# Kernel tuning notes

Measured on AMD Instinct MI355X. Metric: run time of the kernel, lower is better.

## Reference

```python
import jax, jax.numpy as jnp
import numpy as np

B, I, H = 16384, 1024, 1024
LN_EPS = 1e-5


def setup_inputs() -> dict:
    key = jax.random.key(0)
    k1, k2, k3, k4 = jax.random.split(key, 4)
    x = jax.random.normal(k1, (B, I), dtype=jnp.float32)
    h_out = jax.random.normal(k2, (B, H), dtype=jnp.float32)
    cell = jax.random.normal(k3, (B, H), dtype=jnp.float32)
    # nn.Linear(i_size + h, 4*h, bias=False): weight shape [4h, i+h]
    W = jax.random.normal(k4, (4 * H, I + H), dtype=jnp.float32) * (1.0 / np.sqrt(I + H))
    gamma = jnp.ones((4, H), dtype=jnp.float32)
    beta = jnp.zeros((4, H), dtype=jnp.float32)
    return {"x": x, "h_out": h_out, "cell": cell, "W": W, "gamma": gamma, "beta": beta}


def reference(x, h_out, cell, W, gamma, beta):
    # concat + linear -> [B, 4, H]
    cat = jnp.concatenate([x, h_out], axis=-1)               # [B, I+H]
    t = (cat @ W.T).reshape(cat.shape[0], 4, H)              # [B, 4, H]
    # LayerNorm over normalized_shape=(4, H): stats over last two dims
    mu = jnp.mean(t, axis=(-2, -1), keepdims=True)
    var = jnp.mean(jnp.square(t - mu), axis=(-2, -1), keepdims=True)
    handle = (t - mu) * jax.lax.rsqrt(var + LN_EPS) * gamma + beta
    # gates: first 3 slices sigmoid, last slice GELU (exact, eval-mode dropout = identity)
    gates = jax.nn.sigmoid(handle[:, 0:3, :])
    f_gate, i_gate, o_gate = gates[:, 0], gates[:, 1], gates[:, 2]
    h_cand = jax.nn.gelu(handle[:, 3, :], approximate=False)
    new_cell = f_gate * cell + i_gate * h_cand
    new_out = o_gate * new_cell
    return (new_out, new_cell)
```

## Files before the change

### kernel.cpp

```cpp
#include <hip/hip_runtime.h>
#include <stdint.h>

#define B_ROWS 16384
#define IN_DIM 1024
#define H_DIM  1024
#define KDIM   2048
#define NDIM   4096
#define NT     64
#define LN_EPSF 1e-5f

typedef unsigned short u16;
typedef float  f32x4  __attribute__((ext_vector_type(4)));
typedef float  fv4    __attribute__((ext_vector_type(4)));
typedef __bf16 bf16x8 __attribute__((ext_vector_type(8)));
typedef u16    u16x4  __attribute__((ext_vector_type(4)));
typedef u16    u16x8  __attribute__((ext_vector_type(8)));

__device__ __forceinline__ u16 f2bf(float f) {
  unsigned u = __float_as_uint(f);
  u += 0x7FFFu + ((u >> 16) & 1u);
  return (u16)(u >> 16);
}
__device__ __forceinline__ float bf2f(u16 s) {
  return __uint_as_float(((unsigned)s) << 16);
}

#define GLOAD_LDS16(gp, lp) __builtin_amdgcn_global_load_lds( \
    (__attribute__((address_space(1))) void*)(gp),            \
    (__attribute__((address_space(3))) void*)(lp), 16, 0, 0)

__global__ __launch_bounds__(256) void cast_concat(
    const float* __restrict__ x, const float* __restrict__ h,
    u16* __restrict__ cat) {
  int idx = blockIdx.x * 256 + threadIdx.x;
  long base = (long)idx * 8;
  int  c = (int)(base & (KDIM - 1));
  long b = base >> 11;
  const float* src = (c < IN_DIM) ? (x + b * IN_DIM + c)
                                  : (h + b * H_DIM + (c - IN_DIM));
  fv4 v0 = *(const fv4*)(src);
  fv4 v1 = *(const fv4*)(src + 4);
  u16x8 o;
  o[0]=f2bf(v0[0]); o[1]=f2bf(v0[1]); o[2]=f2bf(v0[2]); o[3]=f2bf(v0[3]);
  o[4]=f2bf(v1[0]); o[5]=f2bf(v1[1]); o[6]=f2bf(v1[2]); o[7]=f2bf(v1[3]);
  *(u16x8*)(cat + base) = o;
}

__global__ __launch_bounds__(256) void cast_plain(
    const float* __restrict__ w, u16* __restrict__ wb) {
  int idx = blockIdx.x * 256 + threadIdx.x;
  long base = (long)idx * 8;
  fv4 v0 = *(const fv4*)(w + base);
  fv4 v1 = *(const fv4*)(w + base + 4);
  u16x8 o;
  o[0]=f2bf(v0[0]); o[1]=f2bf(v0[1]); o[2]=f2bf(v0[2]); o[3]=f2bf(v0[3]);
  o[4]=f2bf(v1[0]); o[5]=f2bf(v1[1]); o[6]=f2bf(v1[2]); o[7]=f2bf(v1[3]);
  *(u16x8*)(wb + base) = o;
}


#define BODY(J, CA, CB, NA, NB) do {                                         \
    const int t = tb + (J);                                                  \
    const bool st = (t + 3) < NT;                                            \
    const u16* __restrict__ ab  = &As[(J) & 3][0];                           \
    const u16* __restrict__ bb  = &Bs[(J) & 3][0];                           \
    const u16* __restrict__ abn = &As[((J) + 1) & 3][0];                     \
    const u16* __restrict__ bbn = &Bs[((J) + 1) & 3][0];                     \
    u16* __restrict__ sa = &As[((J) + 3) & 3][0];                            \
    u16* __restrict__ sb = &Bs[((J) + 3) & 3][0];                            \
    if (st) {                                                                \
      GLOAD_LDS16(gA0 + (size_t)(t + 3) * 32, sa + tid * 8);                 \
      GLOAD_LDS16(gA1 + (size_t)(t + 3) * 32, sa + tid * 8 + 4096);          \
    }                                                                        \
    _Pragma("unroll")                                                        \
    for (int i = 0; i < 4; ++i)                                              \
      A47[i] = *(const bf16x8*)(ab + base_a + (4 + i) * 512);                \
    __builtin_amdgcn_sched_barrier(0);                                       \
    __builtin_amdgcn_s_setprio(1);                                           \
    _Pragma("unroll")                                                        \
    for (int m = 0; m < 4; ++m)                                              \
      _Pragma("unroll")                                                      \
      for (int n = 0; n < 4; ++n)                                            \
        acc[m][n] = __builtin_amdgcn_mfma_f32_16x16x32_bf16(                 \
            CA[m], CB[n], acc[m][n], 0, 0, 0);                               \
    __builtin_amdgcn_s_setprio(0);                                           \
    __builtin_amdgcn_sched_barrier(0);                                       \
    if (st) {                                                                \
      GLOAD_LDS16(gB0 + (size_t)(t + 3) * 32, sb + tid * 8);                 \
      GLOAD_LDS16(gB1 + (size_t)(t + 3) * 32, sb + tid * 8 + 4096);          \
    }                                                                        \
    if (t + 1 < NT) {                                                        \
      _Pragma("unroll")                                                      \
      for (int i = 0; i < 4; ++i) {                                          \
        NA[i] = *(const bf16x8*)(abn + base_a + i * 512);                    \
        NB[i] = *(const bf16x8*)(bbn + base_b + i * 512);                    \
      }                                                                      \
    }                                                                        \
    __builtin_amdgcn_sched_barrier(0);                                       \
    __builtin_amdgcn_s_setprio(1);                                           \
    _Pragma("unroll")                                                        \
    for (int m = 0; m < 4; ++m)                                              \
      _Pragma("unroll")                                                      \
      for (int n = 0; n < 4; ++n)                                            \
        acc[4 + m][n] = __builtin_amdgcn_mfma_f32_16x16x32_bf16(             \
            A47[m], CB[n], acc[4 + m][n], 0, 0, 0);                          \
    __builtin_amdgcn_s_setprio(0);                                           \
    __builtin_amdgcn_sched_barrier(0);                                       \
    asm volatile("s_waitcnt vmcnt(4)" ::: "memory");                         \
    __builtin_amdgcn_s_barrier();                                            \
  } while (0)

__global__ __launch_bounds__(512, 2) void gemm_bt(
    const u16* __restrict__ A,
    const u16* __restrict__ Bw,
    u16* __restrict__ C) {
  __shared__ u16 As[4][8192];
  __shared__ u16 Bs[4][8192];

  const int tid  = threadIdx.x;
  const int lane = tid & 63;
  const int wave = tid >> 6;
  const int wm   = wave >> 2;
  const int wn   = wave & 3;
  const int r    = lane & 15;
  const int g    = lane >> 4;

  const int bid = blockIdx.x;
  const int xcd = bid & 7;
  const int k_  = bid >> 3;
  const int row0 = (xcd * 8 + (k_ >> 4)) * 256;
  const int col0 = (k_ & 15) * 256;

  const int tid2 = tid ^ ((tid >> 3) & 7);
  const u16* gA0 = A  + (size_t)(row0 + (tid2 >> 2)) * KDIM + (tid2 & 3) * 8;
  const u16* gA1 = gA0 + (size_t)128 * KDIM;
  const u16* gB0 = Bw + (size_t)(col0 + (tid2 >> 2)) * KDIM + (tid2 & 3) * 8;
  const u16* gB1 = gB0 + (size_t)128 * KDIM;

  const int rswz   = ((r >> 1) & 7) << 3;
  const int base_a = (((wm * 128 + r) * 32) + g * 8) ^ rswz;
  const int base_b = (((wn * 64  + r) * 32) + g * 8) ^ rswz;

  f32x4 acc[8][4] = {};
  bf16x8 XA[4], XB[4], YA[4], YB[4], A47[4];

#pragma unroll
  for (int tt = 0; tt < 3; ++tt) {
    GLOAD_LDS16(gA0 + tt * 32, &As[tt][tid * 8]);
    GLOAD_LDS16(gA1 + tt * 32, &As[tt][tid * 8 + 4096]);
    GLOAD_LDS16(gB0 + tt * 32, &Bs[tt][tid * 8]);
    GLOAD_LDS16(gB1 + tt * 32, &Bs[tt][tid * 8 + 4096]);
  }
  asm volatile("s_waitcnt vmcnt(4)" ::: "memory");
  __builtin_amdgcn_s_barrier();
#pragma unroll
  for (int i = 0; i < 4; ++i) {
    XA[i] = *(const bf16x8*)(&As[0][0] + base_a + i * 512);
    XB[i] = *(const bf16x8*)(&Bs[0][0] + base_b + i * 512);
  }

  for (int u = 0; u < 16; ++u) {
    const int tb = u * 4;
    BODY(0, XA, XB, YA, YB);
    BODY(1, YA, YB, XA, XB);
    BODY(2, XA, XB, YA, YB);
    BODY(3, YA, YB, XA, XB);
  }

#pragma unroll
  for (int m = 0; m < 8; ++m)
#pragma unroll
    for (int n = 0; n < 4; ++n)
#pragma unroll
      for (int q = 0; q < 4; ++q) {
        const int rr = row0 + wm * 128 + m * 16 + g * 4 + q;
        const int cc = col0 + wn * 64 + n * 16 + r;
        C[(size_t)rr * NDIM + cc] = f2bf(acc[m][n][q]);
      }
}

__global__ __launch_bounds__(256) void ln_gates(
    const u16* __restrict__ t,
    const float* __restrict__ cell,
    const float* __restrict__ gamma,
    const float* __restrict__ beta,
    float* __restrict__ out) {
  const int b   = blockIdx.x;
  const int tid = threadIdx.x;
  const int h0  = tid * 4;

  const u16* trow = t + (long)b * NDIM;
  float v[4][4];
#pragma unroll
  for (int gi = 0; gi < 4; ++gi) {
    u16x4 raw = *(const u16x4*)&trow[gi * H_DIM + h0];
#pragma unroll
    for (int j = 0; j < 4; ++j) v[gi][j] = bf2f(raw[j]);
  }

  float s1 = 0.f, s2 = 0.f;
#pragma unroll
  for (int gi = 0; gi < 4; ++gi)
#pragma unroll
    for (int j = 0; j < 4; ++j) { s1 += v[gi][j]; s2 += v[gi][j] * v[gi][j]; }

#pragma unroll
  for (int m = 32; m; m >>= 1) {
    s1 += __shfl_xor(s1, m);
    s2 += __shfl_xor(s2, m);
  }
  __shared__ float red[2][4];
  const int wave = tid >> 6, lane = tid & 63;
  if (lane == 0) { red[0][wave] = s1; red[1][wave] = s2; }
  __syncthreads();
  s1 = red[0][0] + red[0][1] + red[0][2] + red[0][3];
  s2 = red[1][0] + red[1][1] + red[1][2] + red[1][3];

  const float mean  = s1 * (1.f / (float)NDIM);
  const float var   = s2 * (1.f / (float)NDIM) - mean * mean;
  const float scale = rsqrtf(var + LN_EPSF);

  float hd[4][4];
#pragma unroll
  for (int gi = 0; gi < 4; ++gi) {
    fv4 gm = *(const fv4*)&gamma[gi * H_DIM + h0];
    fv4 bt = *(const fv4*)&beta[gi * H_DIM + h0];
#pragma unroll
    for (int j = 0; j < 4; ++j)
      hd[gi][j] = (v[gi][j] - mean) * scale * gm[j] + bt[j];
  }

  fv4 cv = *(const fv4*)&cell[(long)b * H_DIM + h0];
  fv4 no, nc;
#pragma unroll
  for (int j = 0; j < 4; ++j) {
    float fg = 1.f / (1.f + expf(-hd[0][j]));
    float ig = 1.f / (1.f + expf(-hd[1][j]));
    float og = 1.f / (1.f + expf(-hd[2][j]));
    float hc = 0.5f * hd[3][j] * (1.f + erff(hd[3][j] * 0.70710678118654752f));
    float ncell = fg * cv[j] + ig * hc;
    nc[j] = ncell;
    no[j] = og * ncell;
  }
  *(fv4*)&out[(long)b * H_DIM + h0] = no;
  *(fv4*)&out[(long)B_ROWS * H_DIM + (long)b * H_DIM + h0] = nc;
}

extern "C" void kernel_launch(void* const* d_in, const int* in_sizes, int n_in,
                              void* d_out, int out_size, void* d_ws, size_t ws_size,
                              hipStream_t stream) {
  const float* x     = (const float*)d_in[0];
  const float* h     = (const float*)d_in[1];
  const float* cell  = (const float*)d_in[2];
  const float* W     = (const float*)d_in[3];
  const float* gamma = (const float*)d_in[4];
  const float* beta  = (const float*)d_in[5];
  float* out = (float*)d_out;

  const size_t cat_bytes = (size_t)B_ROWS * KDIM * sizeof(u16);
  const size_t w_bytes   = (size_t)NDIM * KDIM * sizeof(u16);
  const size_t t_bytes   = (size_t)B_ROWS * NDIM * sizeof(u16);
  if (ws_size < cat_bytes + w_bytes + t_bytes) return;

  uint8_t* ws = (uint8_t*)d_ws;
  u16* catb = (u16*)ws;
  u16* Wb   = (u16*)(ws + cat_bytes);
  u16* tbuf = (u16*)(ws + cat_bytes + w_bytes);

  cast_concat<<<(B_ROWS * (long)KDIM / 8) / 256, 256, 0, stream>>>(x, h, catb);
  cast_plain<<<(NDIM * (long)KDIM / 8) / 256, 256, 0, stream>>>(W, Wb);

  gemm_bt<<<dim3(1024), 512, 0, stream>>>(catb, Wb, tbuf);

  ln_gates<<<B_ROWS, 256, 0, stream>>>(tbuf, cell, gamma, beta, out);
}
```

Baseline: 382.9 us.

## Use four waves per block with 128x128 wave tiles in bf16 GEMM

The GEMM block shrinks from 512 to 256 threads, and each wave now computes a 128x128 output tile (8x8 MFMA accumulators) instead of 128x64. This raises operand reuse per LDS fragment load and removes the separate A47 reload. Each thread issues four global-to-LDS loads per operand per stage, and the vmcnt waits are adjusted, including a full drain on the tail steps. The cost is much higher register pressure (256 accumulator floats plus 32 fragment vectors) and fewer waves to hide latency, which risks spills or lower occupancy.

New measurement: 435.7 us. 1.14x slower.

```diff
diff --git a/kernel.cpp b/kernel.cpp
--- a/kernel.cpp
+++ b/kernel.cpp
@@ -59,58 +59,57 @@
 }
 
 
-#define BODY(J, CA, CB, NA, NB) do {                                         \
+#define CLUSTER(MB, FA, FB)                                                  \
+  _Pragma("unroll")                                                          \
+  for (int m = 0; m < 4; ++m)                                                \
+    _Pragma("unroll")                                                        \
+    for (int n = 0; n < 8; ++n)                                              \
+      acc[(MB) + m][n] = __builtin_amdgcn_mfma_f32_16x16x32_bf16(            \
+          FA[(MB) + m], FB[n], acc[(MB) + m][n], 0, 0, 0);
+
+#define BODY(J, CA, CB, NA_, NB_) do {                                       \
     const int t = tb + (J);                                                  \
     const bool st = (t + 3) < NT;                                            \
-    const u16* __restrict__ ab  = &As[(J) & 3][0];                           \
-    const u16* __restrict__ bb  = &Bs[(J) & 3][0];                           \
     const u16* __restrict__ abn = &As[((J) + 1) & 3][0];                     \
     const u16* __restrict__ bbn = &Bs[((J) + 1) & 3][0];                     \
     u16* __restrict__ sa = &As[((J) + 3) & 3][0];                            \
     u16* __restrict__ sb = &Bs[((J) + 3) & 3][0];                            \
     if (st) {                                                                \
-      GLOAD_LDS16(gA0 + (size_t)(t + 3) * 32, sa + tid * 8);                 \
-      GLOAD_LDS16(gA1 + (size_t)(t + 3) * 32, sa + tid * 8 + 4096);          \
-    }                                                                        \
-    _Pragma("unroll")                                                        \
-    for (int i = 0; i < 4; ++i)                                              \
-      A47[i] = *(const bf16x8*)(ab + base_a + (4 + i) * 512);                \
+      _Pragma("unroll")                                                      \
+      for (int j = 0; j < 4; ++j)                                            \
+        GLOAD_LDS16(gA[j] + (size_t)(t + 3) * 32, sa + tid * 8 + j * 2048);  \
+    }                                                                        \
+    if (t + 1 < NT) {                                                        \
+      _Pragma("unroll")                                                      \
+      for (int i = 0; i < 8; ++i)                                            \
+        NA_[i] = *(const bf16x8*)(abn + base_a + i * 512);                   \
+    }                                                                        \
     __builtin_amdgcn_sched_barrier(0);                                       \
     __builtin_amdgcn_s_setprio(1);                                           \
-    _Pragma("unroll")                                                        \
-    for (int m = 0; m < 4; ++m)                                              \
-      _Pragma("unroll")                                                      \
-      for (int n = 0; n < 4; ++n)                                            \
-        acc[m][n] = __builtin_amdgcn_mfma_f32_16x16x32_bf16(                 \
-            CA[m], CB[n], acc[m][n], 0, 0, 0);                               \
+    CLUSTER(0, CA, CB)                                                       \
     __builtin_amdgcn_s_setprio(0);                                           \
     __builtin_amdgcn_sched_barrier(0);                                       \
     if (st) {                                                                \
-      GLOAD_LDS16(gB0 + (size_t)(t + 3) * 32, sb + tid * 8);                 \
-      GLOAD_LDS16(gB1 + (size_t)(t + 3) * 32, sb + tid * 8 + 4096);          \
+      _Pragma("unroll")                                                      \
+      for (int j = 0; j < 4; ++j)                                            \
+        GLOAD_LDS16(gB[j] + (size_t)(t + 3) * 32, sb + tid * 8 + j * 2048);  \
     }                                                                        \
     if (t + 1 < NT) {                                                        \
       _Pragma("unroll")                                                      \
-      for (int i = 0; i < 4; ++i) {                                          \
-        NA[i] = *(const bf16x8*)(abn + base_a + i * 512);                    \
-        NB[i] = *(const bf16x8*)(bbn + base_b + i * 512);                    \
-      }                                                                      \
+      for (int i = 0; i < 8; ++i)                                            \
+        NB_[i] = *(const bf16x8*)(bbn + base_b + i * 512);                   \
     }                                                                        \
     __builtin_amdgcn_sched_barrier(0);                                       \
     __builtin_amdgcn_s_setprio(1);                                           \
-    _Pragma("unroll")                                                        \
-    for (int m = 0; m < 4; ++m)                                              \
-      _Pragma("unroll")                                                      \
-      for (int n = 0; n < 4; ++n)                                            \
-        acc[4 + m][n] = __builtin_amdgcn_mfma_f32_16x16x32_bf16(             \
-            A47[m], CB[n], acc[4 + m][n], 0, 0, 0);                          \
+    CLUSTER(4, CA, CB)                                                       \
     __builtin_amdgcn_s_setprio(0);                                           \
     __builtin_amdgcn_sched_barrier(0);                                       \
-    asm volatile("s_waitcnt vmcnt(4)" ::: "memory");                         \
+    if (st) { asm volatile("s_waitcnt vmcnt(8)" ::: "memory"); }             \
+    else    { asm volatile("s_waitcnt vmcnt(0)" ::: "memory"); }             \
     __builtin_amdgcn_s_barrier();                                            \
   } while (0)
 
-__global__ __launch_bounds__(512, 2) void gemm_bt(
+__global__ __launch_bounds__(256, 1) void gemm_bt(
     const u16* __restrict__ A,
     const u16* __restrict__ Bw,
     u16* __restrict__ C) {
@@ -120,8 +119,8 @@
   const int tid  = threadIdx.x;
   const int lane = tid & 63;
   const int wave = tid >> 6;
-  const int wm   = wave >> 2;
-  const int wn   = wave & 3;
+  const int wm   = wave >> 1;
+  const int wn   = wave & 1;
   const int r    = lane & 15;
   const int g    = lane >> 4;
 
@@ -131,30 +130,35 @@
   const int row0 = (xcd * 8 + (k_ >> 4)) * 256;
   const int col0 = (k_ & 15) * 256;
 
-  const int tid2 = tid ^ ((tid >> 3) & 7);
-  const u16* gA0 = A  + (size_t)(row0 + (tid2 >> 2)) * KDIM + (tid2 & 3) * 8;
-  const u16* gA1 = gA0 + (size_t)128 * KDIM;
-  const u16* gB0 = Bw + (size_t)(col0 + (tid2 >> 2)) * KDIM + (tid2 & 3) * 8;
-  const u16* gB1 = gB0 + (size_t)128 * KDIM;
+  const u16* gA[4];
+  const u16* gB[4];
+#pragma unroll
+  for (int j = 0; j < 4; ++j) {
+    const int c  = tid + 256 * j;
+    const int cl = c ^ ((c >> 3) & 7);
+    gA[j] = A  + (size_t)(row0 + (cl >> 2)) * KDIM + (cl & 3) * 8;
+    gB[j] = Bw + (size_t)(col0 + (cl >> 2)) * KDIM + (cl & 3) * 8;
+  }
 
   const int rswz   = ((r >> 1) & 7) << 3;
   const int base_a = (((wm * 128 + r) * 32) + g * 8) ^ rswz;
-  const int base_b = (((wn * 64  + r) * 32) + g * 8) ^ rswz;
-
-  f32x4 acc[8][4] = {};
-  bf16x8 XA[4], XB[4], YA[4], YB[4], A47[4];
+  const int base_b = (((wn * 128 + r) * 32) + g * 8) ^ rswz;
+
+  f32x4 acc[8][8] = {};
+  bf16x8 XA[8], XB[8], YA[8], YB[8];
 
 #pragma unroll
   for (int tt = 0; tt < 3; ++tt) {
-    GLOAD_LDS16(gA0 + tt * 32, &As[tt][tid * 8]);
-    GLOAD_LDS16(gA1 + tt * 32, &As[tt][tid * 8 + 4096]);
-    GLOAD_LDS16(gB0 + tt * 32, &Bs[tt][tid * 8]);
-    GLOAD_LDS16(gB1 + tt * 32, &Bs[tt][tid * 8 + 4096]);
-  }
-  asm volatile("s_waitcnt vmcnt(4)" ::: "memory");
+#pragma unroll
+    for (int j = 0; j < 4; ++j) {
+      GLOAD_LDS16(gA[j] + tt * 32, &As[tt][tid * 8 + j * 2048]);
+      GLOAD_LDS16(gB[j] + tt * 32, &Bs[tt][tid * 8 + j * 2048]);
+    }
+  }
+  asm volatile("s_waitcnt vmcnt(8)" ::: "memory");
   __builtin_amdgcn_s_barrier();
 #pragma unroll
-  for (int i = 0; i < 4; ++i) {
+  for (int i = 0; i < 8; ++i) {
     XA[i] = *(const bf16x8*)(&As[0][0] + base_a + i * 512);
     XB[i] = *(const bf16x8*)(&Bs[0][0] + base_b + i * 512);
   }
@@ -170,11 +174,11 @@
 #pragma unroll
   for (int m = 0; m < 8; ++m)
 #pragma unroll
-    for (int n = 0; n < 4; ++n)
+    for (int n = 0; n < 8; ++n)
 #pragma unroll
       for (int q = 0; q < 4; ++q) {
         const int rr = row0 + wm * 128 + m * 16 + g * 4 + q;
-        const int cc = col0 + wn * 64 + n * 16 + r;
+        const int cc = col0 + wn * 128 + n * 16 + r;
         C[(size_t)rr * NDIM + cc] = f2bf(acc[m][n][q]);
       }
 }
@@ -270,7 +274,7 @@
   cast_concat<<<(B_ROWS * (long)KDIM / 8) / 256, 256, 0, stream>>>(x, h, catb);
   cast_plain<<<(NDIM * (long)KDIM / 8) / 256, 256, 0, stream>>>(W, Wb);
 
-  gemm_bt<<<dim3(1024), 512, 0, stream>>>(catb, Wb, tbuf);
+  gemm_bt<<<dim3(1024), 256, 0, stream>>>(catb, Wb, tbuf);
 
   ln_gates<<<B_ROWS, 256, 0, stream>>>(tbuf, cell, gamma, beta, out);
 }
```

## Prefetch full next A/B fragments before one merged MFMA block per k-step

Applied to the files above, without the earlier changes.

Restructures the GEMM main loop so each k-step issues all four global-to-LDS loads up front, then loads the entire next-step A (8 fragments) and B fragments from LDS before a single 32-MFMA block, instead of splitting MFMAs into two halves interleaved with loads. It removes the separate A47 register set, doubles the A double-buffer register size, and unrolls by two instead of four with runtime buffer indexing. The intent is fewer scheduling barriers and more MFMA work available to hide LDS latency, at the cost of higher register pressure and explicit lgkmcnt(0) waits before each barrier.

Measured after the change: 421.6 us. 1.1x slower.

```diff
diff --git a/kernel.cpp b/kernel.cpp
--- a/kernel.cpp
+++ b/kernel.cpp
@@ -59,54 +59,42 @@
 }
 
 
-#define BODY(J, CA, CB, NA, NB) do {                                         \
-    const int t = tb + (J);                                                  \
+#define BODY(T, CA, CB, NA_, NB_) do {                                       \
+    const int t = (T);                                                       \
     const bool st = (t + 3) < NT;                                            \
-    const u16* __restrict__ ab  = &As[(J) & 3][0];                           \
-    const u16* __restrict__ bb  = &Bs[(J) & 3][0];                           \
-    const u16* __restrict__ abn = &As[((J) + 1) & 3][0];                     \
-    const u16* __restrict__ bbn = &Bs[((J) + 1) & 3][0];                     \
-    u16* __restrict__ sa = &As[((J) + 3) & 3][0];                            \
-    u16* __restrict__ sb = &Bs[((J) + 3) & 3][0];                            \
+    const bool rd = (t + 1) < NT;                                            \
+    u16* __restrict__ sa = &As[0][0] + ((t + 3) & 3) * 8192;                 \
+    u16* __restrict__ sb = &Bs[0][0] + ((t + 3) & 3) * 8192;                 \
+    const u16* __restrict__ na = &As[0][0] + ((t + 1) & 3) * 8192;           \
+    const u16* __restrict__ nb = &Bs[0][0] + ((t + 1) & 3) * 8192;           \
+    const size_t tso = (size_t)(t + 3) * 32;                                 \
     if (st) {                                                                \
-      GLOAD_LDS16(gA0 + (size_t)(t + 3) * 32, sa + tid * 8);                 \
-      GLOAD_LDS16(gA1 + (size_t)(t + 3) * 32, sa + tid * 8 + 4096);          \
+      GLOAD_LDS16(gA0 + tso, sa + tid * 8);                                  \
+      GLOAD_LDS16(gA1 + tso, sa + tid * 8 + 4096);                           \
+      GLOAD_LDS16(gB0 + tso, sb + tid * 8);                                  \
+      GLOAD_LDS16(gB1 + tso, sb + tid * 8 + 4096);                           \
     }                                                                        \
-    _Pragma("unroll")                                                        \
-    for (int i = 0; i < 4; ++i)                                              \
-      A47[i] = *(const bf16x8*)(ab + base_a + (4 + i) * 512);                \
+    if (rd) {                                                                \
+      _Pragma("unroll")                                                      \
+      for (int i = 0; i < 8; ++i)                                            \
+        NA_[i] = *(const bf16x8*)(na + base_a + i * 512);                    \
+      _Pragma("unroll")                                                      \
+      for (int i = 0; i < 4; ++i)                                            \
+        NB_[i] = *(const bf16x8*)(nb + base_b + i * 512);                    \
+    }                                                                        \
     __builtin_amdgcn_sched_barrier(0);                                       \
     __builtin_amdgcn_s_setprio(1);                                           \
     _Pragma("unroll")                                                        \
-    for (int m = 0; m < 4; ++m)                                              \
+    for (int m = 0; m < 8; ++m)                                              \
       _Pragma("unroll")                                                      \
       for (int n = 0; n < 4; ++n)                                            \
         acc[m][n] = __builtin_amdgcn_mfma_f32_16x16x32_bf16(                 \
             CA[m], CB[n], acc[m][n], 0, 0, 0);                               \
     __builtin_amdgcn_s_setprio(0);                                           \
     __builtin_amdgcn_sched_barrier(0);                                       \
-    if (st) {                                                                \
-      GLOAD_LDS16(gB0 + (size_t)(t + 3) * 32, sb + tid * 8);                 \
-      GLOAD_LDS16(gB1 + (size_t)(t + 3) * 32, sb + tid * 8 + 4096);          \
-    }                                                                        \
-    if (t + 1 < NT) {                                                        \
-      _Pragma("unroll")                                                      \
-      for (int i = 0; i < 4; ++i) {                                          \
-        NA[i] = *(const bf16x8*)(abn + base_a + i * 512);                    \
-        NB[i] = *(const bf16x8*)(bbn + base_b + i * 512);                    \
-      }                                                                      \
-    }                                                                        \
+    asm volatile("s_waitcnt lgkmcnt(0)" ::: "memory");                       \
+    asm volatile("s_waitcnt vmcnt(4)" ::: "memory");                         \
     __builtin_amdgcn_sched_barrier(0);                                       \
-    __builtin_amdgcn_s_setprio(1);                                           \
-    _Pragma("unroll")                                                        \
-    for (int m = 0; m < 4; ++m)                                              \
-      _Pragma("unroll")                                                      \
-      for (int n = 0; n < 4; ++n)                                            \
-        acc[4 + m][n] = __builtin_amdgcn_mfma_f32_16x16x32_bf16(             \
-            A47[m], CB[n], acc[4 + m][n], 0, 0, 0);                          \
-    __builtin_amdgcn_s_setprio(0);                                           \
-    __builtin_amdgcn_sched_barrier(0);                                       \
-    asm volatile("s_waitcnt vmcnt(4)" ::: "memory");                         \
     __builtin_amdgcn_s_barrier();                                            \
   } while (0)
 
@@ -142,7 +130,7 @@
   const int base_b = (((wn * 64  + r) * 32) + g * 8) ^ rswz;
 
   f32x4 acc[8][4] = {};
-  bf16x8 XA[4], XB[4], YA[4], YB[4], A47[4];
+  bf16x8 XA[8], XB[4], YA[8], YB[4];
 
 #pragma unroll
   for (int tt = 0; tt < 3; ++tt) {
@@ -154,17 +142,16 @@
   asm volatile("s_waitcnt vmcnt(4)" ::: "memory");
   __builtin_amdgcn_s_barrier();
 #pragma unroll
-  for (int i = 0; i < 4; ++i) {
+  for (int i = 0; i < 8; ++i)
     XA[i] = *(const bf16x8*)(&As[0][0] + base_a + i * 512);
+#pragma unroll
+  for (int i = 0; i < 4; ++i)
     XB[i] = *(const bf16x8*)(&Bs[0][0] + base_b + i * 512);
-  }
-
-  for (int u = 0; u < 16; ++u) {
-    const int tb = u * 4;
-    BODY(0, XA, XB, YA, YB);
-    BODY(1, YA, YB, XA, XB);
-    BODY(2, XA, XB, YA, YB);
-    BODY(3, YA, YB, XA, XB);
+  asm volatile("s_waitcnt lgkmcnt(0)" ::: "memory");
+
+  for (int u = 0; u < NT / 2; ++u) {
+    BODY(2 * u,     XA, XB, YA, YB);
+    BODY(2 * u + 1, YA, YB, XA, XB);
   }
 
 #pragma unroll
```
